# Kernel tuning notes

Hardware: AMD Instinct MI355X
Metric: run time of the kernel (lower is better)

## Reference

```python
import jax, jax.numpy as jnp
import numpy as np

R = 32
EPS = 0.0
BN_EPS = 1e-5


def _voxelize(features, idx):
    # features: [C, N], idx: [N] int32 flat voxel index in [0, R^3)
    V = R * R * R
    pts = features.T  # [N, C]
    sums = jax.ops.segment_sum(pts, idx, num_segments=V)          # [V, C]
    cnts = jax.ops.segment_sum(jnp.ones_like(idx, jnp.float32), idx, num_segments=V)  # [V]
    avg = sums / jnp.maximum(cnts, 1.0)[:, None]
    mx = jax.ops.segment_max(pts, idx, num_segments=V)            # [V, C], -inf for empty
    mx = jnp.where(cnts[:, None] > 0, mx, 0.0)
    return avg, mx, cnts


def reference(features, coords, conv_w, conv_b, bn_gamma, bn_beta, bn_mean, bn_var):
    B, C, N = features.shape
    # --- coordinate normalization (coords detached in original) ---
    nc = coords - jnp.mean(coords, axis=2, keepdims=True)          # [B,3,N]
    norms = jnp.linalg.norm(nc, axis=1, keepdims=True)             # [B,1,N]
    denom = jnp.max(norms, axis=2, keepdims=True) * 2.0 + EPS      # [B,1,1]
    nc = nc / denom + 0.5
    nc = jnp.clip(nc * R, 0.0, R - 1)                              # [B,3,N]
    vox = jnp.round(nc).astype(jnp.int32)                          # [B,3,N]
    idx = vox[:, 0] * (R * R) + vox[:, 1] * R + vox[:, 2]          # [B,N]
    # --- dual scatter reduction (avg + max) per batch ---
    avg, mx, _ = jax.vmap(_voxelize)(features, idx)                # [B, V, C] each
    fea = jnp.concatenate([mx, avg], axis=-1)                      # [B, V, 2C]
    # --- 1x1 Conv3d == channel matmul ---
    y = jnp.einsum('bvc,oc->bvo', fea, conv_w) + conv_b            # [B, V, C]
    # --- BatchNorm3d (eval mode) ---
    y = (y - bn_mean) * (bn_gamma / jnp.sqrt(bn_var + BN_EPS)) + bn_beta
    # --- Swish ---
    y = y * jax.nn.sigmoid(y)
    out = jnp.transpose(y, (0, 2, 1)).reshape(B, C, R, R, R)
    return out, nc


def setup_inputs() -> dict:
    key = jax.random.key(0)
    ks = jax.random.split(key, 8)
    B, C, N = 8, 240, 16384
    return {
        'features': jax.random.normal(ks[0], (B, C, N), jnp.float32),
        'coords': jax.random.normal(ks[1], (B, 3, N), jnp.float32),
        'conv_w': jax.random.normal(ks[2], (C, 2 * C), jnp.float32) * 0.05,
        'conv_b': jax.random.normal(ks[3], (C,), jnp.float32) * 0.05,
        'bn_gamma': jnp.ones((C,), jnp.float32),
        'bn_beta': jnp.zeros((C,), jnp.float32),
        'bn_mean': jnp.zeros((C,), jnp.float32),
        'bn_var': jax.random.uniform(ks[4], (C,), jnp.float32, 0.5, 1.5),
    }
```

## Files before the change

kernel.cpp:

```cpp
#include <hip/hip_runtime.h>
#include <math.h>

#define RR 32
#define V 32768
#define C 240
#define N 16384
#define B 8
#define K2C 480
#define GZ 16
#define NGRP 2048
#define FPAD 488
#define EBUF 512

typedef __attribute__((ext_vector_type(8))) short bf16x8;
typedef __attribute__((ext_vector_type(4))) float f32x4;

__device__ __forceinline__ unsigned short f2bf(float x) {
    unsigned u = __float_as_uint(x);
    u += 0x7fffu + ((u >> 16) & 1u);
    return (unsigned short)(u >> 16);
}

__global__ __launch_bounds__(256) void prep_kernel(const float* __restrict__ feat,
                                                   unsigned short* __restrict__ featT,
                                                   const float* __restrict__ coords,
                                                   float* __restrict__ stats,
                                                   int* __restrict__ hist,
                                                   int* __restrict__ wlcnt,
                                                   const float* __restrict__ w,
                                                   unsigned short* __restrict__ w_bf) {
    __shared__ float t[C][33];
    int blk = blockIdx.x;
    int tid = threadIdx.x;
    if (blk < 4096) {
        int bx = blk & 511, b = blk >> 9;
        int n0 = bx * 32;
        int l = tid;
        const float* fb = feat + (size_t)b * C * N;
        unsigned short* fTb = featT + (size_t)b * N * C;
        int nl = l & 31, cs = l >> 5;
#pragma unroll
        for (int p = 0; p < 30; ++p) {
            int c = p * 8 + cs;
            t[c][nl] = fb[(size_t)c * N + n0 + nl];
        }
        __syncthreads();
        int ci = l & 127;
        int nh = l >> 7;
#pragma unroll
        for (int p = 0; p < 16; ++p) {
            int n = 2 * p + nh;
            if (ci < 120) {
                unsigned lo = f2bf(t[2 * ci][n]);
                unsigned hi = f2bf(t[2 * ci + 1][n]);
                *(unsigned*)&fTb[(size_t)(n0 + n) * C + 2 * ci] = lo | (hi << 16);
            }
        }
        return;
    }
    if (blk < 4352) {
        int tt = (blk - 4096) * 256 + tid;
        int4 z4 = {0, 0, 0, 0};
        ((int4*)hist)[tt] = z4;
        if (tt < 57600) {
            unsigned lo = f2bf(w[2 * tt]);
            unsigned hi = f2bf(w[2 * tt + 1]);
            ((unsigned*)w_bf)[tt] = lo | (hi << 16);
        }
        if (tt < 2 * B) wlcnt[tt] = 0;
        return;
    }
    int b = blk - 4352;
    const float* cb = coords + (size_t)b * 3 * N;
    __shared__ float red[256];
    float m[3];
    for (int d = 0; d < 3; ++d) {
        float s = 0.f;
        for (int n = tid; n < N; n += 256) s += cb[d * N + n];
        red[tid] = s; __syncthreads();
        for (int w2 = 128; w2 > 0; w2 >>= 1) { if (tid < w2) red[tid] += red[tid + w2]; __syncthreads(); }
        m[d] = red[0] / (float)N;
        __syncthreads();
    }
    float mx = 0.f;
    for (int n = tid; n < N; n += 256) {
        float dx = cb[0 * N + n] - m[0];
        float dy = cb[1 * N + n] - m[1];
        float dz = cb[2 * N + n] - m[2];
        mx = fmaxf(mx, dx * dx + dy * dy + dz * dz);
    }
    red[tid] = mx; __syncthreads();
    for (int w2 = 128; w2 > 0; w2 >>= 1) { if (tid < w2) red[tid] = fmaxf(red[tid], red[tid + w2]); __syncthreads(); }
    if (tid == 0) {
        stats[b * 4 + 0] = m[0];
        stats[b * 4 + 1] = m[1];
        stats[b * 4 + 2] = m[2];
        stats[b * 4 + 3] = 2.f * sqrtf(red[0]);
    }
}

__global__ __launch_bounds__(256) void nc_idx_kernel(const float* __restrict__ coords,
                                                     const float* __restrict__ stats,
                                                     float* __restrict__ nc_out,
                                                     int* __restrict__ idxbuf,
                                                     int* __restrict__ hist) {
    int t = blockIdx.x * 256 + threadIdx.x;
    int b = t >> 14;
    int n = t & (N - 1);
    float denom = stats[b * 4 + 3];
    int v[3];
#pragma unroll
    for (int d = 0; d < 3; ++d) {
        float x = coords[((size_t)b * 3 + d) * N + n];
        float t0 = (x - stats[b * 4 + d]) / denom + 0.5f;
        t0 = t0 * (float)RR;
        t0 = fminf(fmaxf(t0, 0.f), (float)(RR - 1));
        nc_out[((size_t)b * 3 + d) * N + n] = t0;
        v[d] = (int)rintf(t0);
    }
    int iv = v[0] * (RR * RR) + v[1] * RR + v[2];
    idxbuf[t] = iv;
    atomicAdd(hist + b * V + iv, 1);
}

__global__ __launch_bounds__(1024) void prefix_kernel(const int* __restrict__ hist,
                                                      int* __restrict__ starts,
                                                      int* __restrict__ cursor,
                                                      int* __restrict__ wl,
                                                      int* __restrict__ wlcnt) {
    __shared__ int part[1024];
    int b = blockIdx.x, t = threadIdx.x;
    int base = b * V + t * 32;
    const int4* hp = (const int4*)(hist + base);
    int4 h[8];
#pragma unroll
    for (int j = 0; j < 8; ++j) h[j] = hp[j];
    int pcA = h[0].x + h[0].y + h[0].z + h[0].w + h[1].x + h[1].y + h[1].z + h[1].w
            + h[2].x + h[2].y + h[2].z + h[2].w + h[3].x + h[3].y + h[3].z + h[3].w;
    int pcB = h[4].x + h[4].y + h[4].z + h[4].w + h[5].x + h[5].y + h[5].z + h[5].w
            + h[6].x + h[6].y + h[6].z + h[6].w + h[7].x + h[7].y + h[7].z + h[7].w;
    int s = pcA + pcB;
    if (pcA > 0) { int p = atomicAdd(wlcnt + b, 1); wl[b * NGRP + p] = 2 * t; }
    if (pcB > 0) { int p = atomicAdd(wlcnt + b, 1); wl[b * NGRP + p] = 2 * t + 1; }
    if (pcA == 0 && pcB == 0) { int q = atomicAdd(wlcnt + B + b, 1); wl[b * NGRP + NGRP - 1 - q] = (2 * t) | 0x10000; }
    else if (pcA == 0)        { int q = atomicAdd(wlcnt + B + b, 1); wl[b * NGRP + NGRP - 1 - q] = 2 * t; }
    else if (pcB == 0)        { int q = atomicAdd(wlcnt + B + b, 1); wl[b * NGRP + NGRP - 1 - q] = 2 * t + 1; }
    part[t] = s; __syncthreads();
    for (int off = 1; off < 1024; off <<= 1) {
        int x = (t >= off) ? part[t - off] : 0;
        __syncthreads();
        part[t] += x;
        __syncthreads();
    }
    int run = part[t] - s;
    int4* sp = (int4*)(starts + base);
    int4* cp = (int4*)(cursor + base);
#pragma unroll
    for (int j = 0; j < 8; ++j) {
        int4 o;
        o.x = run; run += h[j].x;
        o.y = run; run += h[j].y;
        o.z = run; run += h[j].z;
        o.w = run; run += h[j].w;
        sp[j] = o; cp[j] = o;
    }
}

__global__ __launch_bounds__(256) void plist_kernel(const int* __restrict__ idxbuf,
                                                    int* __restrict__ cursor,
                                                    int* __restrict__ ptlist) {
    int t = blockIdx.x * 256 + threadIdx.x;
    int b = t >> 14;
    int n = t & (N - 1);
    int iv = idxbuf[t];
    int pos = atomicAdd(cursor + b * V + iv, 1);
    ptlist[(b << 14) + pos] = (n << 5) | (iv & 31);
}

#define PF2(U, Z0, Z1, basei)                                               \
    {                                                                       \
        Z0 = 0u; Z1 = 0u;                                                   \
        _Pragma("unroll")                                                   \
        for (int j = 0; j < 16; ++j) {                                      \
            int idx = basei + j; idx = (idx < mm) ? idx : mm - 1;           \
            int e = ebg[idx];                                               \
            U[j] = *(const unsigned*)&fT[(size_t)(e >> 5) * C + cc2];       \
            unsigned zz = (unsigned)(e & 15);                               \
            if (j < 8) Z0 |= zz << (4 * j); else Z1 |= zz << (4 * (j - 8)); \
        }                                                                   \
    }

#define PR2(U, Z0, Z1, basei)                                               \
    {                                                                       \
        _Pragma("unroll")                                                   \
        for (int j = 0; j < 16; ++j) {                                      \
            if (basei + j < mm) {                                           \
                int zj = (int)(((j < 8 ? Z0 : Z1) >> (4 * (j & 7))) & 15u); \
                if (zj != curz) {                                           \
                    if (curz >= 0) {                                        \
                        float rc = rcp_s[rb + curz];                        \
                        *(unsigned*)&fea_s[rb + curz][cc2] =                \
                            (unsigned)f2bf(mx0) | ((unsigned)f2bf(mx1) << 16); \
                        *(unsigned*)&fea_s[rb + curz][C + cc2] =            \
                            (unsigned)f2bf(s0 * rc) | ((unsigned)f2bf(s1 * rc) << 16); \
                    }                                                       \
                    curz = zj; s0 = s1 = 0.f; mx0 = mx1 = -INFINITY;        \
                }                                                           \
                unsigned u = U[j];                                          \
                float flo = __uint_as_float(u << 16);                       \
                float fhi = __uint_as_float(u & 0xffff0000u);               \
                s0 += flo; s1 += fhi;                                       \
                mx0 = fmaxf(mx0, flo); mx1 = fmaxf(mx1, fhi);               \
            }                                                               \
        }                                                                   \
    }

__global__ __launch_bounds__(256, 4) void column_kernel(
    const unsigned short* __restrict__ featT,
    const int* __restrict__ ptlist,
    const int* __restrict__ starts,
    const int* __restrict__ hist,
    const unsigned short* __restrict__ w_bf,
    const float* __restrict__ cbias, const float* __restrict__ gamma,
    const float* __restrict__ beta, const float* __restrict__ mean,
    const float* __restrict__ var,
    const int* __restrict__ wl, const int* __restrict__ wlcnt,
    float* __restrict__ out) {
    const int bx = blockIdx.x, b = blockIdx.y;
    const int nw = wlcnt[b];
    const int npair = (nw + 1) >> 1;
    const int ntot = npair + wlcnt[B + b];
    if (bx >= ntot) return;
    const bool isfill = (bx >= npair);
    const int tid = threadIdx.x;
    float* outb = out + (size_t)b * C * V;

    __shared__ float A_s[C], B_s[C], y0_s[C], rcp_s[2 * GZ];
    __shared__ unsigned short fea_s[2 * GZ][FPAD];
    __shared__ int cnt_s[2 * GZ];
    __shared__ int ebuf0[EBUF], ebuf1[EBUF];

    int wle0, wle1 = 0;
    bool has1 = false;
    if (isfill) {
        wle0 = wl[b * NGRP + NGRP - 1 - (bx - npair)];
    } else {
        wle0 = wl[b * NGRP + 2 * bx];
        has1 = (2 * bx + 1) < nw;
        wle1 = has1 ? wl[b * NGRP + 2 * bx + 1] : wle0;
    }
    const int v00 = (wle0 & 0xffff) * GZ;
    const int v01 = (wle1 & 0xffff) * GZ;

    if (tid < C) {
        float sc = gamma[tid] * rsqrtf(var[tid] + 1e-5f);
        A_s[tid] = sc;
        float b0 = (cbias[tid] - mean[tid]) * sc + beta[tid];
        B_s[tid] = b0;
        y0_s[tid] = b0 / (1.f + __expf(-b0));
    }
    if (!isfill && tid < 2 * GZ) {
        int c0;
        if (tid < GZ) c0 = hist[b * V + v00 + tid];
        else          c0 = has1 ? hist[b * V + v01 + (tid - GZ)] : 0;
        cnt_s[tid] = c0;
        rcp_s[tid] = 1.f / (float)max(c0, 1);
    }
    __syncthreads();

    if (isfill) {
        if (wle0 >> 16) {
            for (int i = tid; i < C * 8; i += 256) {
                int o = i >> 3, q = i & 7;
                float y = y0_s[o];
                float4 f4 = {y, y, y, y};
                *(float4*)&outb[(size_t)o * V + v00 + q * 4] = f4;
            }
        } else {
            for (int i = tid; i < C * 4; i += 256) {
                int o = i >> 2, q = i & 3;
                float y = y0_s[o];
                float4 f4 = {y, y, y, y};
                *(float4*)&outb[(size_t)o * V + v00 + q * 4] = f4;
            }
        }
        return;
    }

    int pc0 = 0, pc1 = 0;
#pragma unroll
    for (int z = 0; z < GZ; ++z) { pc0 += cnt_s[z]; pc1 += cnt_s[GZ + z]; }

    for (int i = tid; i < 2 * GZ * FPAD / 2; i += 256) ((unsigned*)fea_s)[i] = 0u;

    const unsigned short* fT = featT + (size_t)b * N * C;
    const int lane = tid & 63, wave = tid >> 6;
    const int grp = wave >> 1;
    const int rb = grp << 4;
    const int cc = tid & 127;
    const int cc2 = cc << 1;
    const bool act = cc < 120;
    const int* pl0 = ptlist + (b << 14) + starts[b * V + v00];
    const int* pl1 = ptlist + (b << 14) + starts[b * V + v01];
    const int* ebg = grp ? ebuf1 : ebuf0;

    float s0 = 0.f, s1 = 0.f, mx0 = -INFINITY, mx1 = -INFINITY;
    int curz = -1;
    const int pcmax = max(pc0, pc1);
    for (int base = 0; base < pcmax; base += EBUF) {
        int mm0 = min(EBUF, pc0 - base);
        int mm1 = min(EBUF, pc1 - base);
        __syncthreads();
        for (int i = tid; i < mm0; i += 256) ebuf0[i] = pl0[base + i];
        for (int i = tid; i < mm1; i += 256) ebuf1[i] = pl1[base + i];
        __syncthreads();
        int mm = grp ? mm1 : mm0;
        if (act && mm > 0) {
            unsigned uA[16], uB[16];
            unsigned zA0 = 0, zA1 = 0, zB0 = 0, zB1 = 0;
            PF2(uA, zA0, zA1, 0);
            for (int i0 = 0; i0 < mm; i0 += 32) {
                if (i0 + 16 < mm) PF2(uB, zB0, zB1, i0 + 16);
                PR2(uA, zA0, zA1, i0);
                if (i0 + 32 < mm) PF2(uA, zA0, zA1, i0 + 32);
                PR2(uB, zB0, zB1, i0 + 16);
            }
        }
    }
    if (act && curz >= 0) {
        float rc = rcp_s[rb + curz];
        *(unsigned*)&fea_s[rb + curz][cc2] = (unsigned)f2bf(mx0) | ((unsigned)f2bf(mx1) << 16);
        *(unsigned*)&fea_s[rb + curz][C + cc2] = (unsigned)f2bf(s0 * rc) | ((unsigned)f2bf(s1 * rc) << 16);
    }
    __syncthreads();

    const int mcnt = (wave == 3) ? 3 : 4;
    const int zl = lane & 15;
    const int koff = (lane >> 4) * 8;
    const int rbase = (lane >> 4) * 4;

    f32x4 acc0[4], acc1[4];
#pragma unroll
    for (int i = 0; i < 4; ++i) { acc0[i] = (f32x4){0.f, 0.f, 0.f, 0.f}; acc1[i] = (f32x4){0.f, 0.f, 0.f, 0.f}; }

#pragma unroll
    for (int kc = 0; kc < 15; ++kc) {
        const int kg = kc * 32 + koff;
        bf16x8 bfr0 = *(const bf16x8*)&fea_s[zl][kg];
        bf16x8 bfr1 = *(const bf16x8*)&fea_s[GZ + zl][kg];
        const unsigned short* wp = w_bf + (size_t)(wave * 64 + zl) * K2C + kg;
#pragma unroll
        for (int mt = 0; mt < 4; ++mt) {
            if (mt < mcnt) {
                bf16x8 afr = *(const bf16x8*)(wp + (size_t)mt * 16 * K2C);
                acc0[mt] = __builtin_amdgcn_mfma_f32_16x16x32_bf16(afr, bfr0, acc0[mt], 0, 0, 0);
                acc1[mt] = __builtin_amdgcn_mfma_f32_16x16x32_bf16(afr, bfr1, acc1[mt], 0, 0, 0);
            }
        }
    }

    const int vv0 = v00 + zl, vv1 = v01 + zl;
#pragma unroll
    for (int mt = 0; mt < 4; ++mt) {
        if (mt < mcnt) {
#pragma unroll
            for (int r = 0; r < 4; ++r) {
                int o = (wave * 4 + mt) * 16 + rbase + r;
                float y = acc0[mt][r] * A_s[o] + B_s[o];
                y = y / (1.f + __expf(-y));
                outb[(size_t)o * V + vv0] = y;
                if (has1) {
                    float y1 = acc1[mt][r] * A_s[o] + B_s[o];
                    y1 = y1 / (1.f + __expf(-y1));
                    outb[(size_t)o * V + vv1] = y1;
                }
            }
        }
    }
}

extern "C" void kernel_launch(void* const* d_in, const int* in_sizes, int n_in,
                              void* d_out, int out_size, void* d_ws, size_t ws_size,
                              hipStream_t stream) {
    const float* features = (const float*)d_in[0];
    const float* coords   = (const float*)d_in[1];
    const float* conv_w   = (const float*)d_in[2];
    const float* conv_b   = (const float*)d_in[3];
    const float* gamma    = (const float*)d_in[4];
    const float* beta     = (const float*)d_in[5];
    const float* mean     = (const float*)d_in[6];
    const float* var      = (const float*)d_in[7];

    float* out    = (float*)d_out;
    float* nc_out = out + (size_t)B * C * V;

    char* ws = (char*)d_ws;
    size_t off = 0;
    auto carve = [&](size_t bytes) { char* p = ws + off; off += (bytes + 255) & ~(size_t)255; return p; };
    int*            hist   = (int*)carve((size_t)B * V * 4);
    float*          stats  = (float*)carve(B * 4 * 4);
    int*            idxbuf = (int*)carve((size_t)B * N * 4);
    int*            starts = (int*)carve((size_t)B * V * 4);
    int*            cursor = (int*)carve((size_t)B * V * 4);
    int*            ptlist = (int*)carve((size_t)B * N * 4);
    int*            wl     = (int*)carve((size_t)B * NGRP * 4);
    int*            wlcnt  = (int*)carve((size_t)2 * B * 4);
    unsigned short* w_bf   = (unsigned short*)carve((size_t)C * K2C * 2);
    unsigned short* featT  = (unsigned short*)carve((size_t)B * N * C * 2);
    (void)off;

    prep_kernel<<<4360, 256, 0, stream>>>(features, featT, coords, stats, hist, wlcnt, conv_w, w_bf);
    nc_idx_kernel<<<(B * N) / 256, 256, 0, stream>>>(coords, stats, nc_out, idxbuf, hist);
    prefix_kernel<<<B, 1024, 0, stream>>>(hist, starts, cursor, wl, wlcnt);
    plist_kernel<<<(B * N) / 256, 256, 0, stream>>>(idxbuf, cursor, ptlist);
    column_kernel<<<dim3(NGRP, B), 256, 0, stream>>>(
        featT, ptlist, starts, hist, w_bf,
        conv_b, gamma, beta, mean, var, wl, wlcnt, out);
    (void)in_sizes; (void)n_in; (void)out_size;
}
```

Before: 554.9 us.

## Convert column kernel to persistent blocks with global atomic work queues

Replaces the per-batch 2D grid of column blocks with 1024 persistent blocks that pull column pairs from a single global worklist via an atomic counter, then drain a separate fill list. Compute pairs can now span batches, and the per-block setup (BN constants) is amortized over many work items, removing many early-exit blocks. The cost is an atomic grab plus two block barriers per item, and possible load imbalance at the tail.

```diff
diff --git a/kernel.cpp b/kernel.cpp
--- a/kernel.cpp
+++ b/kernel.cpp
@@ -26,7 +26,7 @@
                                                    const float* __restrict__ coords,
                                                    float* __restrict__ stats,
                                                    int* __restrict__ hist,
-                                                   int* __restrict__ wlcnt,
+                                                   int* __restrict__ ctrs,
                                                    const float* __restrict__ w,
                                                    unsigned short* __restrict__ w_bf) {
     __shared__ float t[C][33];
@@ -67,7 +67,7 @@
             unsigned hi = f2bf(w[2 * tt + 1]);
             ((unsigned*)w_bf)[tt] = lo | (hi << 16);
         }
-        if (tt < 2 * B) wlcnt[tt] = 0;
+        if (tt < 4) ctrs[tt] = 0;
         return;
     }
     int b = blk - 4352;
@@ -126,8 +126,9 @@
 __global__ __launch_bounds__(1024) void prefix_kernel(const int* __restrict__ hist,
                                                       int* __restrict__ starts,
                                                       int* __restrict__ cursor,
-                                                      int* __restrict__ wl,
-                                                      int* __restrict__ wlcnt) {
+                                                      int* __restrict__ gwl,
+                                                      int* __restrict__ gfl,
+                                                      int* __restrict__ ctrs) {
     __shared__ int part[1024];
     int b = blockIdx.x, t = threadIdx.x;
     int base = b * V + t * 32;
@@ -140,11 +141,11 @@
     int pcB = h[4].x + h[4].y + h[4].z + h[4].w + h[5].x + h[5].y + h[5].z + h[5].w
             + h[6].x + h[6].y + h[6].z + h[6].w + h[7].x + h[7].y + h[7].z + h[7].w;
     int s = pcA + pcB;
-    if (pcA > 0) { int p = atomicAdd(wlcnt + b, 1); wl[b * NGRP + p] = 2 * t; }
-    if (pcB > 0) { int p = atomicAdd(wlcnt + b, 1); wl[b * NGRP + p] = 2 * t + 1; }
-    if (pcA == 0 && pcB == 0) { int q = atomicAdd(wlcnt + B + b, 1); wl[b * NGRP + NGRP - 1 - q] = (2 * t) | 0x10000; }
-    else if (pcA == 0)        { int q = atomicAdd(wlcnt + B + b, 1); wl[b * NGRP + NGRP - 1 - q] = 2 * t; }
-    else if (pcB == 0)        { int q = atomicAdd(wlcnt + B + b, 1); wl[b * NGRP + NGRP - 1 - q] = 2 * t + 1; }
+    if (pcA > 0) { int p = atomicAdd(ctrs + 0, 1); gwl[p] = (b << 11) | (2 * t); }
+    if (pcB > 0) { int p = atomicAdd(ctrs + 0, 1); gwl[p] = (b << 11) | (2 * t + 1); }
+    if (pcA == 0 && pcB == 0) { int q = atomicAdd(ctrs + 1, 1); gfl[q] = 0x4000 | (b << 11) | (2 * t); }
+    else if (pcA == 0)        { int q = atomicAdd(ctrs + 1, 1); gfl[q] = (b << 11) | (2 * t); }
+    else if (pcB == 0)        { int q = atomicAdd(ctrs + 1, 1); gfl[q] = (b << 11) | (2 * t + 1); }
     part[t] = s; __syncthreads();
     for (int off = 1; off < 1024; off <<= 1) {
         int x = (t >= off) ? part[t - off] : 0;
@@ -182,8 +183,8 @@
         Z0 = 0u; Z1 = 0u;                                                   \
         _Pragma("unroll")                                                   \
         for (int j = 0; j < 16; ++j) {                                      \
-            int idx = basei + j; idx = (idx < mm) ? idx : mm - 1;           \
-            int e = ebg[idx];                                               \
+            int idx2 = basei + j; idx2 = (idx2 < mm) ? idx2 : mm - 1;       \
+            int e = ebg[idx2];                                              \
             U[j] = *(const unsigned*)&fT[(size_t)(e >> 5) * C + cc2];       \
             unsigned zz = (unsigned)(e & 15);                               \
             if (j < 8) Z0 |= zz << (4 * j); else Z1 |= zz << (4 * (j - 8)); \
@@ -224,33 +225,16 @@
     const float* __restrict__ cbias, const float* __restrict__ gamma,
     const float* __restrict__ beta, const float* __restrict__ mean,
     const float* __restrict__ var,
-    const int* __restrict__ wl, const int* __restrict__ wlcnt,
+    const int* __restrict__ gwl, const int* __restrict__ gfl,
+    int* __restrict__ ctrs,
     float* __restrict__ out) {
-    const int bx = blockIdx.x, b = blockIdx.y;
-    const int nw = wlcnt[b];
-    const int npair = (nw + 1) >> 1;
-    const int ntot = npair + wlcnt[B + b];
-    if (bx >= ntot) return;
-    const bool isfill = (bx >= npair);
     const int tid = threadIdx.x;
-    float* outb = out + (size_t)b * C * V;
 
     __shared__ float A_s[C], B_s[C], y0_s[C], rcp_s[2 * GZ];
     __shared__ unsigned short fea_s[2 * GZ][FPAD];
     __shared__ int cnt_s[2 * GZ];
     __shared__ int ebuf0[EBUF], ebuf1[EBUF];
-
-    int wle0, wle1 = 0;
-    bool has1 = false;
-    if (isfill) {
-        wle0 = wl[b * NGRP + NGRP - 1 - (bx - npair)];
-    } else {
-        wle0 = wl[b * NGRP + 2 * bx];
-        has1 = (2 * bx + 1) < nw;
-        wle1 = has1 ? wl[b * NGRP + 2 * bx + 1] : wle0;
-    }
-    const int v00 = (wle0 & 0xffff) * GZ;
-    const int v01 = (wle1 & 0xffff) * GZ;
+    __shared__ int grab_s;
 
     if (tid < C) {
         float sc = gamma[tid] * rsqrtf(var[tid] + 1e-5f);
@@ -259,121 +243,146 @@
         B_s[tid] = b0;
         y0_s[tid] = b0 / (1.f + __expf(-b0));
     }
-    if (!isfill && tid < 2 * GZ) {
-        int c0;
-        if (tid < GZ) c0 = hist[b * V + v00 + tid];
-        else          c0 = has1 ? hist[b * V + v01 + (tid - GZ)] : 0;
-        cnt_s[tid] = c0;
-        rcp_s[tid] = 1.f / (float)max(c0, 1);
-    }
-    __syncthreads();
-
-    if (isfill) {
-        if (wle0 >> 16) {
-            for (int i = tid; i < C * 8; i += 256) {
-                int o = i >> 3, q = i & 7;
-                float y = y0_s[o];
-                float4 f4 = {y, y, y, y};
-                *(float4*)&outb[(size_t)o * V + v00 + q * 4] = f4;
-            }
-        } else {
-            for (int i = tid; i < C * 4; i += 256) {
-                int o = i >> 2, q = i & 3;
-                float y = y0_s[o];
-                float4 f4 = {y, y, y, y};
-                *(float4*)&outb[(size_t)o * V + v00 + q * 4] = f4;
-            }
-        }
-        return;
-    }
-
-    int pc0 = 0, pc1 = 0;
-#pragma unroll
-    for (int z = 0; z < GZ; ++z) { pc0 += cnt_s[z]; pc1 += cnt_s[GZ + z]; }
-
-    for (int i = tid; i < 2 * GZ * FPAD / 2; i += 256) ((unsigned*)fea_s)[i] = 0u;
-
-    const unsigned short* fT = featT + (size_t)b * N * C;
+    const int ncomp = ctrs[0];
+    const int nfill = ctrs[1];
+
     const int lane = tid & 63, wave = tid >> 6;
     const int grp = wave >> 1;
     const int rb = grp << 4;
     const int cc = tid & 127;
     const int cc2 = cc << 1;
     const bool act = cc < 120;
-    const int* pl0 = ptlist + (b << 14) + starts[b * V + v00];
-    const int* pl1 = ptlist + (b << 14) + starts[b * V + v01];
-    const int* ebg = grp ? ebuf1 : ebuf0;
-
-    float s0 = 0.f, s1 = 0.f, mx0 = -INFINITY, mx1 = -INFINITY;
-    int curz = -1;
-    const int pcmax = max(pc0, pc1);
-    for (int base = 0; base < pcmax; base += EBUF) {
-        int mm0 = min(EBUF, pc0 - base);
-        int mm1 = min(EBUF, pc1 - base);
-        __syncthreads();
-        for (int i = tid; i < mm0; i += 256) ebuf0[i] = pl0[base + i];
-        for (int i = tid; i < mm1; i += 256) ebuf1[i] = pl1[base + i];
-        __syncthreads();
-        int mm = grp ? mm1 : mm0;
-        if (act && mm > 0) {
-            unsigned uA[16], uB[16];
-            unsigned zA0 = 0, zA1 = 0, zB0 = 0, zB1 = 0;
-            PF2(uA, zA0, zA1, 0);
-            for (int i0 = 0; i0 < mm; i0 += 32) {
-                if (i0 + 16 < mm) PF2(uB, zB0, zB1, i0 + 16);
-                PR2(uA, zA0, zA1, i0);
-                if (i0 + 32 < mm) PF2(uA, zA0, zA1, i0 + 32);
-                PR2(uB, zB0, zB1, i0 + 16);
-            }
-        }
-    }
-    if (act && curz >= 0) {
-        float rc = rcp_s[rb + curz];
-        *(unsigned*)&fea_s[rb + curz][cc2] = (unsigned)f2bf(mx0) | ((unsigned)f2bf(mx1) << 16);
-        *(unsigned*)&fea_s[rb + curz][C + cc2] = (unsigned)f2bf(s0 * rc) | ((unsigned)f2bf(s1 * rc) << 16);
-    }
-    __syncthreads();
-
     const int mcnt = (wave == 3) ? 3 : 4;
     const int zl = lane & 15;
     const int koff = (lane >> 4) * 8;
     const int rbase = (lane >> 4) * 4;
 
-    f32x4 acc0[4], acc1[4];
-#pragma unroll
-    for (int i = 0; i < 4; ++i) { acc0[i] = (f32x4){0.f, 0.f, 0.f, 0.f}; acc1[i] = (f32x4){0.f, 0.f, 0.f, 0.f}; }
-
-#pragma unroll
-    for (int kc = 0; kc < 15; ++kc) {
-        const int kg = kc * 32 + koff;
-        bf16x8 bfr0 = *(const bf16x8*)&fea_s[zl][kg];
-        bf16x8 bfr1 = *(const bf16x8*)&fea_s[GZ + zl][kg];
-        const unsigned short* wp = w_bf + (size_t)(wave * 64 + zl) * K2C + kg;
+    for (;;) {
+        __syncthreads();
+        if (tid == 0) grab_s = atomicAdd(ctrs + 2, 2);
+        __syncthreads();
+        const int idx = grab_s;
+        if (idx >= ncomp) break;
+        const int e0 = gwl[idx];
+        const bool has1 = (idx + 1) < ncomp;
+        const int e1 = has1 ? gwl[idx + 1] : e0;
+        const int b0i = (e0 >> 11) & 7, b1i = (e1 >> 11) & 7;
+        const int v00 = (e0 & 0x7ff) * GZ, v01 = (e1 & 0x7ff) * GZ;
+
+        if (tid < GZ) {
+            int c0 = hist[b0i * V + v00 + tid];
+            cnt_s[tid] = c0; rcp_s[tid] = 1.f / (float)max(c0, 1);
+        } else if (tid < 2 * GZ) {
+            int c0 = hist[b1i * V + v01 + (tid - GZ)];
+            cnt_s[tid] = c0; rcp_s[tid] = 1.f / (float)max(c0, 1);
+        }
+        for (int i = tid; i < 2 * GZ * FPAD / 2; i += 256) ((unsigned*)fea_s)[i] = 0u;
+        __syncthreads();
+
+        int pc0 = 0, pc1 = 0;
+#pragma unroll
+        for (int z = 0; z < GZ; ++z) { pc0 += cnt_s[z]; pc1 += cnt_s[GZ + z]; }
+
+        const unsigned short* fT = featT + (size_t)(grp ? b1i : b0i) * N * C;
+        const int* pl0 = ptlist + (b0i << 14) + starts[b0i * V + v00];
+        const int* pl1 = ptlist + (b1i << 14) + starts[b1i * V + v01];
+        const int* ebg = grp ? ebuf1 : ebuf0;
+
+        float s0 = 0.f, s1 = 0.f, mx0 = -INFINITY, mx1 = -INFINITY;
+        int curz = -1;
+        const int pcmax = max(pc0, pc1);
+        for (int base = 0; base < pcmax; base += EBUF) {
+            int mm0 = min(EBUF, pc0 - base);
+            int mm1 = min(EBUF, pc1 - base);
+            __syncthreads();
+            for (int i = tid; i < mm0; i += 256) ebuf0[i] = pl0[base + i];
+            for (int i = tid; i < mm1; i += 256) ebuf1[i] = pl1[base + i];
+            __syncthreads();
+            int mm = grp ? mm1 : mm0;
+            if (act && mm > 0) {
+                unsigned uA[16], uB[16];
+                unsigned zA0 = 0, zA1 = 0, zB0 = 0, zB1 = 0;
+                PF2(uA, zA0, zA1, 0);
+                for (int i0 = 0; i0 < mm; i0 += 32) {
+                    if (i0 + 16 < mm) PF2(uB, zB0, zB1, i0 + 16);
+                    PR2(uA, zA0, zA1, i0);
+                    if (i0 + 32 < mm) PF2(uA, zA0, zA1, i0 + 32);
+                    PR2(uB, zB0, zB1, i0 + 16);
+                }
+            }
+        }
+        if (act && curz >= 0) {
+            float rc = rcp_s[rb + curz];
+            *(unsigned*)&fea_s[rb + curz][cc2] = (unsigned)f2bf(mx0) | ((unsigned)f2bf(mx1) << 16);
+            *(unsigned*)&fea_s[rb + curz][C + cc2] = (unsigned)f2bf(s0 * rc) | ((unsigned)f2bf(s1 * rc) << 16);
+        }
+        __syncthreads();
+
+        f32x4 acc0[4], acc1[4];
+#pragma unroll
+        for (int i = 0; i < 4; ++i) { acc0[i] = (f32x4){0.f, 0.f, 0.f, 0.f}; acc1[i] = (f32x4){0.f, 0.f, 0.f, 0.f}; }
+
+#pragma unroll
+        for (int kc = 0; kc < 15; ++kc) {
+            const int kg = kc * 32 + koff;
+            bf16x8 bfr0 = *(const bf16x8*)&fea_s[zl][kg];
+            bf16x8 bfr1 = *(const bf16x8*)&fea_s[GZ + zl][kg];
+            const unsigned short* wp = w_bf + (size_t)(wave * 64 + zl) * K2C + kg;
+#pragma unroll
+            for (int mt = 0; mt < 4; ++mt) {
+                if (mt < mcnt) {
+                    bf16x8 afr = *(const bf16x8*)(wp + (size_t)mt * 16 * K2C);
+                    acc0[mt] = __builtin_amdgcn_mfma_f32_16x16x32_bf16(afr, bfr0, acc0[mt], 0, 0, 0);
+                    acc1[mt] = __builtin_amdgcn_mfma_f32_16x16x32_bf16(afr, bfr1, acc1[mt], 0, 0, 0);
+                }
+            }
+        }
+
+        float* outb0 = out + (size_t)b0i * C * V;
+        float* outb1 = out + (size_t)b1i * C * V;
+        const int vv0 = v00 + zl, vv1 = v01 + zl;
 #pragma unroll
         for (int mt = 0; mt < 4; ++mt) {
             if (mt < mcnt) {
-                bf16x8 afr = *(const bf16x8*)(wp + (size_t)mt * 16 * K2C);
-                acc0[mt] = __builtin_amdgcn_mfma_f32_16x16x32_bf16(afr, bfr0, acc0[mt], 0, 0, 0);
-                acc1[mt] = __builtin_amdgcn_mfma_f32_16x16x32_bf16(afr, bfr1, acc1[mt], 0, 0, 0);
-            }
-        }
-    }
-
-    const int vv0 = v00 + zl, vv1 = v01 + zl;
-#pragma unroll
-    for (int mt = 0; mt < 4; ++mt) {
-        if (mt < mcnt) {
-#pragma unroll
-            for (int r = 0; r < 4; ++r) {
-                int o = (wave * 4 + mt) * 16 + rbase + r;
-                float y = acc0[mt][r] * A_s[o] + B_s[o];
-                y = y / (1.f + __expf(-y));
-                outb[(size_t)o * V + vv0] = y;
-                if (has1) {
-                    float y1 = acc1[mt][r] * A_s[o] + B_s[o];
-                    y1 = y1 / (1.f + __expf(-y1));
-                    outb[(size_t)o * V + vv1] = y1;
+#pragma unroll
+                for (int r = 0; r < 4; ++r) {
+                    int o = (wave * 4 + mt) * 16 + rbase + r;
+                    float y = acc0[mt][r] * A_s[o] + B_s[o];
+                    y = y / (1.f + __expf(-y));
+                    outb0[(size_t)o * V + vv0] = y;
+                    if (has1) {
+                        float y1 = acc1[mt][r] * A_s[o] + B_s[o];
+                        y1 = y1 / (1.f + __expf(-y1));
+                        outb1[(size_t)o * V + vv1] = y1;
+                    }
                 }
+            }
+        }
+    }
+
+    for (;;) {
+        __syncthreads();
+        if (tid == 0) grab_s = atomicAdd(ctrs + 3, 1);
+        __syncthreads();
+        const int idx = grab_s;
+        if (idx >= nfill) break;
+        const int e = gfl[idx];
+        const int bb = (e >> 11) & 7;
+        const int v0 = (e & 0x7ff) * GZ;
+        float* outb = out + (size_t)bb * C * V;
+        if (e & 0x4000) {
+            for (int i = tid; i < C * 8; i += 256) {
+                int o = i >> 3, q = i & 7;
+                float y = y0_s[o];
+                float4 f4 = {y, y, y, y};
+                *(float4*)&outb[(size_t)o * V + v0 + q * 4] = f4;
+            }
+        } else {
+            for (int i = tid; i < C * 4; i += 256) {
+                int o = i >> 2, q = i & 3;
+                float y = y0_s[o];
+                float4 f4 = {y, y, y, y};
+                *(float4*)&outb[(size_t)o * V + v0 + q * 4] = f4;
             }
         }
     }
@@ -403,18 +412,19 @@
     int*            starts = (int*)carve((size_t)B * V * 4);
     int*            cursor = (int*)carve((size_t)B * V * 4);
     int*            ptlist = (int*)carve((size_t)B * N * 4);
-    int*            wl     = (int*)carve((size_t)B * NGRP * 4);
-    int*            wlcnt  = (int*)carve((size_t)2 * B * 4);
+    int*            gwl    = (int*)carve((size_t)B * NGRP * 4);
+    int*            gfl    = (int*)carve((size_t)B * NGRP * 4);
+    int*            ctrs   = (int*)carve(4 * 4);
     unsigned short* w_bf   = (unsigned short*)carve((size_t)C * K2C * 2);
     unsigned short* featT  = (unsigned short*)carve((size_t)B * N * C * 2);
     (void)off;
 
-    prep_kernel<<<4360, 256, 0, stream>>>(features, featT, coords, stats, hist, wlcnt, conv_w, w_bf);
+    prep_kernel<<<4360, 256, 0, stream>>>(features, featT, coords, stats, hist, ctrs, conv_w, w_bf);
     nc_idx_kernel<<<(B * N) / 256, 256, 0, stream>>>(coords, stats, nc_out, idxbuf, hist);
-    prefix_kernel<<<B, 1024, 0, stream>>>(hist, starts, cursor, wl, wlcnt);
+    prefix_kernel<<<B, 1024, 0, stream>>>(hist, starts, cursor, gwl, gfl, ctrs);
     plist_kernel<<<(B * N) / 256, 256, 0, stream>>>(idxbuf, cursor, ptlist);
-    column_kernel<<<dim3(NGRP, B), 256, 0, stream>>>(
+    column_kernel<<<1024, 256, 0, stream>>>(
         featT, ptlist, starts, hist, w_bf,
-        conv_b, gamma, beta, mean, var, wl, wlcnt, out);
+        conv_b, gamma, beta, mean, var, gwl, gfl, ctrs, out);
     (void)in_sizes; (void)n_in; (void)out_size;
 }
```

New measurement: 656.6 us. 18.3% more time.
